# Kernel tuning notes

Hardware: AMD Instinct MI355X
Metric: run time of the kernel (lower is better)

Reference implementation:

```python
import jax, jax.numpy as jnp
import numpy as np

V, H_BASE, D, L, K = 32000, 4096, 512, 2, 4
B = 64

def setup_inputs() -> dict:
    key = jax.random.key(0)
    ks = jax.random.split(key, 12)
    s = 0.02
    return {
        "hidden_state": jax.random.normal(ks[0], (B, H_BASE), jnp.float32),
        "in_proj_w": jax.random.normal(ks[1], (D, H_BASE), jnp.float32) * s,
        "in_proj_b": jnp.zeros((D,), jnp.float32),
        "w_ih0": jax.random.normal(ks[2], (3 * D, D), jnp.float32) * s,
        "w_hh0": jax.random.normal(ks[3], (3 * D, D), jnp.float32) * s,
        "b_ih0": jax.random.normal(ks[4], (3 * D,), jnp.float32) * s,
        "b_hh0": jax.random.normal(ks[5], (3 * D,), jnp.float32) * s,
        "w_ih1": jax.random.normal(ks[6], (3 * D, D), jnp.float32) * s,
        "w_hh1": jax.random.normal(ks[7], (3 * D, D), jnp.float32) * s,
        "b_ih1": jax.random.normal(ks[8], (3 * D,), jnp.float32) * s,
        "b_hh1": jax.random.normal(ks[9], (3 * D,), jnp.float32) * s,
        "embed": jax.random.normal(ks[10], (V, D), jnp.float32) * s,
        "out_w": jax.random.normal(ks[11], (V, D), jnp.float32) * s,
    }

def _gru_cell(x, h, w_ih, w_hh, b_ih, b_hh):
    # PyTorch GRU gate order: r, z, n
    gi = x @ w_ih.T + b_ih  # [B, 3D]
    gh = h @ w_hh.T + b_hh
    ir, iz, inn = jnp.split(gi, 3, axis=-1)
    hr, hz, hn = jnp.split(gh, 3, axis=-1)
    r = jax.nn.sigmoid(ir + hr)
    z = jax.nn.sigmoid(iz + hz)
    n = jnp.tanh(inn + r * hn)
    return (1.0 - z) * n + z * h

def reference(hidden_state, in_proj_w, in_proj_b, w_ih0, w_hh0, b_ih0, b_hh0,
              w_ih1, w_hh1, b_ih1, b_hh1, embed, out_w):
    b = hidden_state.shape[0]
    h0 = hidden_state @ in_proj_w.T + in_proj_b  # [B, D]
    h_l0 = h0
    h_l1 = h0
    x = jnp.zeros((b, in_proj_w.shape[0]), hidden_state.dtype)
    all_logits = []
    for _ in range(K):
        h_l0 = _gru_cell(x, h_l0, w_ih0, w_hh0, b_ih0, b_hh0)
        h_l1 = _gru_cell(h_l0, h_l1, w_ih1, w_hh1, b_ih1, b_hh1)
        logits = h_l1 @ out_w.T  # [B, V]
        all_logits.append(logits)
        x = embed[jnp.argmax(logits, axis=-1)]  # greedy next-token embed
    return jnp.stack(all_logits, axis=1)  # [B, K, V]
```

## Files before the change

### kernel.cpp

```cpp
#include <hip/hip_runtime.h>
#include <math.h>


typedef __attribute__((ext_vector_type(8))) short short8;
typedef __attribute__((ext_vector_type(4))) float f32x4;

__device__ __forceinline__ unsigned short f2bf_rne(float x) {
    unsigned u = __float_as_uint(x);
    unsigned r = (u + 0x7fffu + ((u >> 16) & 1u)) >> 16;
    return (unsigned short)r;
}
__device__ __forceinline__ void split2(float x, unsigned short& hi, unsigned short& lo) {
    unsigned u = __float_as_uint(x);
    hi = (unsigned short)(u >> 16);
    float r = x - __uint_as_float(u & 0xffff0000u);
    lo = f2bf_rne(r);
}

__device__ __forceinline__ void store_plane(unsigned short* hiP, unsigned short* loP,
                                            int m, int d, float v) {
    int s = d >> 6, cl = (d >> 3) & 7, e = d & 7;
    int off = m * 512 + s * 64 + ((cl ^ (m & 7)) * 8) + e;
    unsigned short hi, lo; split2(v, hi, lo);
    hiP[off] = hi; loP[off] = lo;
}

__device__ __forceinline__ void gload16(const void* g, void* lds) {
    __builtin_amdgcn_global_load_lds(
        (const __attribute__((address_space(1))) unsigned int*)g,
        (__attribute__((address_space(3))) unsigned int*)lds, 16, 0, 0);
}

__device__ __forceinline__ void split_w_body(
    const float* __restrict__ W, unsigned short* __restrict__ H,
    unsigned short* __restrict__ L, size_t g, int kclog)
{
    int n  = (int)(g >> kclog);
    int c8 = (int)g & ((1 << kclog) - 1);
    const float* src = W + g * 8;
    float4 v0 = *(const float4*)src;
    float4 v1 = *(const float4*)(src + 4);
    unsigned short h[8], l[8];
    split2(v0.x,h[0],l[0]); split2(v0.y,h[1],l[1]); split2(v0.z,h[2],l[2]); split2(v0.w,h[3],l[3]);
    split2(v1.x,h[4],l[4]); split2(v1.y,h[5],l[5]); split2(v1.z,h[6],l[6]); split2(v1.w,h[7],l[7]);
    uint4 ph = make_uint4((unsigned)h[0]|((unsigned)h[1]<<16), (unsigned)h[2]|((unsigned)h[3]<<16),
                          (unsigned)h[4]|((unsigned)h[5]<<16), (unsigned)h[6]|((unsigned)h[7]<<16));
    uint4 pl = make_uint4((unsigned)l[0]|((unsigned)l[1]<<16), (unsigned)l[2]|((unsigned)l[3]<<16),
                          (unsigned)l[4]|((unsigned)l[5]<<16), (unsigned)l[6]|((unsigned)l[7]<<16));
    int nt = n >> 7, row = n & 127;
    int ksi = c8 >> 3;
    int slot = (c8 & 7) ^ (row & 7);
    int tpr = 1 << (kclog - 3);
    size_t off = ((size_t)(nt * tpr + ksi) * 128 + row) * 64 + slot * 8;
    *(uint4*)(H + off) = ph;
    *(uint4*)(L + off) = pl;
}

__global__ __launch_bounds__(256) void k_split_W(
    const float* __restrict__ W, unsigned short* __restrict__ H,
    unsigned short* __restrict__ L, int kclog)
{
    size_t g = (size_t)blockIdx.x * 256 + threadIdx.x;
    split_w_body(W, H, L, g, kclog);
}

__global__ __launch_bounds__(256) void k_split_gw(
    const float* __restrict__ w0, const float* __restrict__ w1,
    const float* __restrict__ w2, const float* __restrict__ w3,
    unsigned short* __restrict__ H, unsigned short* __restrict__ L)
{
    int mat = blockIdx.y;
    const float* W = mat == 0 ? w0 : mat == 1 ? w1 : mat == 2 ? w2 : w3;
    size_t g = (size_t)blockIdx.x * 256 + threadIdx.x;
    split_w_body(W, H + (size_t)mat * 786432, L + (size_t)mat * 786432, g, 6);
}

__global__ __launch_bounds__(256) void k_split_A(
    const float* __restrict__ hidden, char* __restrict__ hidH, char* __restrict__ hidL)
{
    int g = blockIdx.x * 256 + threadIdx.x;
    int m = g >> 9;
    int cc = g & 511;
    int s = cc >> 3, cl = cc & 7;
    const float* src = hidden + m * 4096 + cc * 8;
    float4 v0 = *(const float4*)src;
    float4 v1 = *(const float4*)(src + 4);
    unsigned short h[8], l[8];
    split2(v0.x,h[0],l[0]); split2(v0.y,h[1],l[1]); split2(v0.z,h[2],l[2]); split2(v0.w,h[3],l[3]);
    split2(v1.x,h[4],l[4]); split2(v1.y,h[5],l[5]); split2(v1.z,h[6],l[6]); split2(v1.w,h[7],l[7]);
    uint4 ph = make_uint4((unsigned)h[0]|((unsigned)h[1]<<16), (unsigned)h[2]|((unsigned)h[3]<<16),
                          (unsigned)h[4]|((unsigned)h[5]<<16), (unsigned)h[6]|((unsigned)h[7]<<16));
    uint4 pl = make_uint4((unsigned)l[0]|((unsigned)l[1]<<16), (unsigned)l[2]|((unsigned)l[3]<<16),
                          (unsigned)l[4]|((unsigned)l[5]<<16), (unsigned)l[6]|((unsigned)l[7]<<16));
    int off = m * 8192 + s * 128 + ((cl ^ (m & 7)) * 16);
    *(uint4*)(hidH + off) = ph;
    *(uint4*)(hidL + off) = pl;
}

__device__ __forceinline__ void mfma_core(
    const unsigned short* __restrict__ AsH0, const unsigned short* __restrict__ AsL0,
    const unsigned short* __restrict__ BsH0, const unsigned short* __restrict__ BsL0,
    int wv, int lr, int lh, f32x4* acc)
{
#pragma unroll
    for (int kk2 = 0; kk2 < 2; ++kk2) {
        int aoff = lr * 64 + (((kk2 * 4 + lh) ^ (lr & 7)) * 8);
        short8 ah[4], al[4];
#pragma unroll
        for (int mt = 0; mt < 4; ++mt) {
            ah[mt] = *(const short8*)(AsH0 + mt * 1024 + aoff);
            al[mt] = *(const short8*)(AsL0 + mt * 1024 + aoff);
        }
        int brow = wv * 16 + lr;
        int boff = brow * 64 + (((kk2 * 4 + lh) ^ (brow & 7)) * 8);
        short8 bh = *(const short8*)(BsH0 + boff);
        short8 bl = *(const short8*)(BsL0 + boff);
#pragma unroll
        for (int mt = 0; mt < 4; ++mt) {
            acc[mt] = __builtin_amdgcn_mfma_f32_16x16x32_bf16(ah[mt], bh, acc[mt], 0, 0, 0);
            acc[mt] = __builtin_amdgcn_mfma_f32_16x16x32_bf16(ah[mt], bl, acc[mt], 0, 0, 0);
            acc[mt] = __builtin_amdgcn_mfma_f32_16x16x32_bf16(al[mt], bh, acc[mt], 0, 0, 0);
        }
    }
}

__device__ __forceinline__ void epilogue_write(
    float* __restrict__ C, int ldc, int n0, int wv, int lr, int lh, const f32x4* acc)
{
#pragma unroll
    for (int mt = 0; mt < 4; ++mt)
#pragma unroll
        for (int i = 0; i < 4; ++i) {
            int mm = mt * 16 + lh * 4 + i;
            C[mm * ldc + n0 + wv * 16 + lr] = acc[mt][i];
        }
}

__device__ __forceinline__ void mfma_gemm(
    const char* __restrict__ AH, const char* __restrict__ AL, int AstrideB, int akk0,
    const unsigned short* __restrict__ BH, const unsigned short* __restrict__ BL,
    size_t btileU, int nk,
    float* __restrict__ C, int ldc, int n0,
    unsigned short (*AsH)[4096], unsigned short (*AsL)[4096],
    unsigned short (*BsH)[8192], unsigned short (*BsL)[8192])
{
    const int tid  = threadIdx.x;
    const int wv   = tid >> 6;
    const int lane = tid & 63;
    const int lr   = lane & 15;
    const int lh   = lane >> 4;
    const int m    = tid >> 3;
    const int cp   = tid & 7;

    f32x4 acc[4];
#pragma unroll
    for (int i = 0; i < 4; ++i) acc[i] = (f32x4){0.f, 0.f, 0.f, 0.f};

    auto stage = [&](int t, int p) {
        const int ka = (akk0 + t * 64) * 2;
        gload16(AH + m * AstrideB + ka + cp * 16, (char*)AsH[p] + wv * 1024);
        gload16(AL + m * AstrideB + ka + cp * 16, (char*)AsL[p] + wv * 1024);
        const char* bH = (const char*)BH + (btileU + (size_t)t * 8192) * 2;
        const char* bL = (const char*)BL + (btileU + (size_t)t * 8192) * 2;
        gload16(bH + wv * 2048 +        lane * 16, (char*)BsH[p] + wv * 2048);
        gload16(bH + wv * 2048 + 1024 + lane * 16, (char*)BsH[p] + wv * 2048 + 1024);
        gload16(bL + wv * 2048 +        lane * 16, (char*)BsL[p] + wv * 2048);
        gload16(bL + wv * 2048 + 1024 + lane * 16, (char*)BsL[p] + wv * 2048 + 1024);
    };

    stage(0, 0);
    __syncthreads();

    for (int t = 0; t < nk; ++t) {
        const int p = t & 1;
        if (t + 1 < nk) stage(t + 1, p ^ 1);
        mfma_core(AsH[p], AsL[p], BsH[p], BsL[p], wv, lr, lh, acc);
        __syncthreads();
    }

    epilogue_write(C, ldc, n0, wv, lr, lh, acc);
}

#define DECLARE_LDS() \
    __shared__ alignas(16) unsigned short AsH[2][4096]; \
    __shared__ alignas(16) unsigned short AsL[2][4096]; \
    __shared__ alignas(16) unsigned short BsH[2][8192]; \
    __shared__ alignas(16) unsigned short BsL[2][8192];

__global__ __launch_bounds__(512) void k_inproj(
    const char* __restrict__ hidH, const char* __restrict__ hidL,
    const unsigned short* __restrict__ WH, const unsigned short* __restrict__ WL,
    float* __restrict__ part)
{
    DECLARE_LDS();
    int nt = blockIdx.x & 3;
    int ks = blockIdx.x >> 2;
    mfma_gemm(hidH, hidL, 8192, ks * 256,
              WH, WL, (size_t)(nt * 64 + ks * 4) * 8192, 4,
              part + ks * 32768, 512, nt * 128,
              AsH, AsL, BsH, BsL);
}

__global__ __launch_bounds__(256) void k_reduce_inproj(
    const float* __restrict__ part, const float* __restrict__ bias,
    float* __restrict__ hA, float* __restrict__ hB,
    unsigned short* hAH, unsigned short* hAL,
    unsigned short* hBH, unsigned short* hBL,
    unsigned short* xH,  unsigned short* xL)
{
    int i = blockIdx.x * 256 + threadIdx.x;
    int b = i >> 9;
    int d = i & 511;
    float s = bias[d];
#pragma unroll
    for (int ks = 0; ks < 16; ++ks) s += part[ks * 32768 + i];
    hA[i] = s;
    hB[i] = s;
    store_plane(hAH, hAL, b, d, s);
    store_plane(hBH, hBL, b, d, s);
    store_plane(xH,  xL,  b, d, 0.f);
}

__global__ __launch_bounds__(512) void k_gates(
    const char* __restrict__ xH, const char* __restrict__ xL,
    const char* __restrict__ hH, const char* __restrict__ hL,
    const unsigned short* __restrict__ gwH, const unsigned short* __restrict__ gwL,
    int layer, float* __restrict__ gip, float* __restrict__ ghp)
{
    DECLARE_LDS();
    int bx  = blockIdx.x;
    int nt  = bx % 12;
    int ks  = (bx / 12) & 3;
    int mat = bx / 48;
    const char* AH = mat ? hH : xH;
    const char* AL = mat ? hL : xL;
    float* C = (mat ? ghp : gip) + ks * 98304;
    size_t btile = ((size_t)(layer * 2 + mat) * 96 + nt * 8 + ks * 2) * 8192;
    mfma_gemm(AH, AL, 1024, ks * 128,
              gwH, gwL, btile, 2,
              C, 1536, nt * 128,
              AsH, AsL, BsH, BsL);
}

__global__ __launch_bounds__(256) void k_combine(
    const float* __restrict__ gip, const float* __restrict__ ghp,
    const float* __restrict__ b_ih, const float* __restrict__ b_hh,
    float* __restrict__ h, unsigned short* hH, unsigned short* hL)
{
    int i = blockIdx.x * 256 + threadIdx.x;
    int b = i >> 9;
    int d = i & 511;
    int base = b * 1536 + d;
    float ir = b_ih[d], iz = b_ih[d + 512], inn = b_ih[d + 1024];
    float hr = b_hh[d], hz = b_hh[d + 512], hn = b_hh[d + 1024];
#pragma unroll
    for (int ks = 0; ks < 4; ++ks) {
        const float* gi = gip + ks * 98304 + base;
        const float* gh = ghp + ks * 98304 + base;
        ir  += gi[0];    iz += gi[512];  inn += gi[1024];
        hr  += gh[0];    hz += gh[512];  hn  += gh[1024];
    }
    float r = 1.f / (1.f + expf(-(ir + hr)));
    float z = 1.f / (1.f + expf(-(iz + hz)));
    float n = tanhf(inn + r * hn);
    float hv = (1.f - z) * n + z * h[i];
    h[i] = hv;
    store_plane(hH, hL, b, d, hv);
}

__global__ __launch_bounds__(256) void k_logits(
    const char* __restrict__ hBH, const char* __restrict__ hBL,
    const float* __restrict__ out_w,
    float* __restrict__ out, int step,
    float* __restrict__ pval, int* __restrict__ pidx)
{
    __shared__ alignas(16) unsigned short AsH[2][4096];
    __shared__ alignas(16) unsigned short AsL[2][4096];
    __shared__ alignas(16) unsigned short BsH[2][4096];
    __shared__ alignas(16) unsigned short BsL[2][4096];

    const int tid  = threadIdx.x;
    const int wv   = tid >> 6;
    const int lane = tid & 63;
    const int lr   = lane & 15;
    const int lh   = lane >> 4;
    const int bx   = blockIdx.x;
    const int n0   = bx * 64;

    const int ar1 = wv * 16 + (lane >> 3);
    const int acp = lane & 7;
    auto stageA = [&](int kaB, int p) {
        gload16(hBH + ar1 * 1024 + kaB + acp * 16,       (char*)AsH[p] + wv * 2048);
        gload16(hBH + (ar1 + 8) * 1024 + kaB + acp * 16, (char*)AsH[p] + wv * 2048 + 1024);
        gload16(hBL + ar1 * 1024 + kaB + acp * 16,       (char*)AsL[p] + wv * 2048);
        gload16(hBL + (ar1 + 8) * 1024 + kaB + acp * 16, (char*)AsL[p] + wv * 2048 + 1024);
    };

    const int bn = tid >> 2, bq = tid & 3;
    const float* Wb = out_w + (size_t)(n0 + bn) * 512 + bq * 16;
    const int wo0 = bn * 64 + (((2 * bq)     ^ (bn & 7)) * 8);
    const int wo1 = bn * 64 + (((2 * bq + 1) ^ (bn & 7)) * 8);

    float4 r0, r1, r2, r3;
    auto loadB = [&](int t) {
        const float* s = Wb + t * 64;
        r0 = *(const float4*)s;       r1 = *(const float4*)(s + 4);
        r2 = *(const float4*)(s + 8); r3 = *(const float4*)(s + 12);
    };
    auto writeB = [&](int p) {
        unsigned short h[16], l[16];
        split2(r0.x,h[0],l[0]);   split2(r0.y,h[1],l[1]);   split2(r0.z,h[2],l[2]);   split2(r0.w,h[3],l[3]);
        split2(r1.x,h[4],l[4]);   split2(r1.y,h[5],l[5]);   split2(r1.z,h[6],l[6]);   split2(r1.w,h[7],l[7]);
        split2(r2.x,h[8],l[8]);   split2(r2.y,h[9],l[9]);   split2(r2.z,h[10],l[10]); split2(r2.w,h[11],l[11]);
        split2(r3.x,h[12],l[12]); split2(r3.y,h[13],l[13]); split2(r3.z,h[14],l[14]); split2(r3.w,h[15],l[15]);
        *(uint4*)(BsH[p] + wo0) = make_uint4(
            (unsigned)h[0]|((unsigned)h[1]<<16),  (unsigned)h[2]|((unsigned)h[3]<<16),
            (unsigned)h[4]|((unsigned)h[5]<<16),  (unsigned)h[6]|((unsigned)h[7]<<16));
        *(uint4*)(BsH[p] + wo1) = make_uint4(
            (unsigned)h[8]|((unsigned)h[9]<<16),  (unsigned)h[10]|((unsigned)h[11]<<16),
            (unsigned)h[12]|((unsigned)h[13]<<16),(unsigned)h[14]|((unsigned)h[15]<<16));
        *(uint4*)(BsL[p] + wo0) = make_uint4(
            (unsigned)l[0]|((unsigned)l[1]<<16),  (unsigned)l[2]|((unsigned)l[3]<<16),
            (unsigned)l[4]|((unsigned)l[5]<<16),  (unsigned)l[6]|((unsigned)l[7]<<16));
        *(uint4*)(BsL[p] + wo1) = make_uint4(
            (unsigned)l[8]|((unsigned)l[9]<<16),  (unsigned)l[10]|((unsigned)l[11]<<16),
            (unsigned)l[12]|((unsigned)l[13]<<16),(unsigned)l[14]|((unsigned)l[15]<<16));
    };

    f32x4 acc[4];
#pragma unroll
    for (int i = 0; i < 4; ++i) acc[i] = (f32x4){0.f, 0.f, 0.f, 0.f};

    loadB(0);
    stageA(0, 0);
    writeB(0);
    __syncthreads();
#pragma unroll
    for (int t = 0; t < 8; ++t) {
        const int p = t & 1;
        if (t < 7) { loadB(t + 1); stageA((t + 1) * 128, p ^ 1); }
        mfma_core(AsH[p], AsL[p], BsH[p], BsL[p], wv, lr, lh, acc);
        if (t < 7) writeB(p ^ 1);
        __syncthreads();
    }

    epilogue_write(out + step * 32000, 128000, n0, wv, lr, lh, acc);

    float* sv = (float*)&AsH[0][0];
    int*   sc = (int*)&AsL[0][0];
#pragma unroll
    for (int mt = 0; mt < 4; ++mt)
#pragma unroll
        for (int i = 0; i < 4; ++i) {
            float v = acc[mt][i];
            int   c = n0 + wv * 16 + lr;
#pragma unroll
            for (int msk = 1; msk < 16; msk <<= 1) {
                float ov = __shfl_xor(v, msk, 64);
                int   oc = __shfl_xor(c, msk, 64);
                if (ov > v || (ov == v && oc < c)) { v = ov; c = oc; }
            }
            if (lr == 0) {
                int row = mt * 16 + lh * 4 + i;
                sv[wv * 64 + row] = v;
                sc[wv * 64 + row] = c;
            }
        }
    __syncthreads();
    if (tid < 64) {
        float v = sv[tid]; int c = sc[tid];
#pragma unroll
        for (int w = 1; w < 4; ++w) {
            float ov = sv[w * 64 + tid]; int oc = sc[w * 64 + tid];
            if (ov > v || (ov == v && oc < c)) { v = ov; c = oc; }
        }
        pval[bx * 64 + tid] = v;
        pidx[bx * 64 + tid] = c;
    }
}

__global__ __launch_bounds__(256) void k_reduce_embed(
    const float* __restrict__ pval, const int* __restrict__ pidx,
    const float* __restrict__ embed, unsigned short* xH, unsigned short* xL)
{
    __shared__ float sv[256];
    __shared__ int   sc[256];
    const int b = blockIdx.x;
    const int tid = threadIdx.x;
    float v = pval[tid * 64 + b];
    int   c = pidx[tid * 64 + b];
    if (tid + 256 < 500) {
        float ov = pval[(tid + 256) * 64 + b];
        int   oc = pidx[(tid + 256) * 64 + b];
        if (ov > v || (ov == v && oc < c)) { v = ov; c = oc; }
    }
    sv[tid] = v; sc[tid] = c;
    __syncthreads();
    for (int s = 128; s > 0; s >>= 1) {
        if (tid < s) {
            float ov = sv[tid + s]; int oc = sc[tid + s];
            if (ov > sv[tid] || (ov == sv[tid] && oc < sc[tid])) { sv[tid] = ov; sc[tid] = oc; }
        }
        __syncthreads();
    }
    int tok = sc[0];
    for (int j = tid; j < 512; j += 256)
        store_plane(xH, xL, b, j, embed[(size_t)tok * 512 + j]);
}

extern "C" void kernel_launch(void* const* d_in, const int* in_sizes, int n_in,
                              void* d_out, int out_size, void* d_ws, size_t ws_size,
                              hipStream_t stream)
{
    const float* hidden = (const float*)d_in[0];
    const float* in_w   = (const float*)d_in[1];
    const float* in_b   = (const float*)d_in[2];
    const float* w_ih0  = (const float*)d_in[3];
    const float* w_hh0  = (const float*)d_in[4];
    const float* b_ih0  = (const float*)d_in[5];
    const float* b_hh0  = (const float*)d_in[6];
    const float* w_ih1  = (const float*)d_in[7];
    const float* w_hh1  = (const float*)d_in[8];
    const float* b_ih1  = (const float*)d_in[9];
    const float* b_hh1  = (const float*)d_in[10];
    const float* embed  = (const float*)d_in[11];
    const float* out_w  = (const float*)d_in[12];
    float* out = (float*)d_out;
    char*  ws  = (char*)d_ws;

    float* hA  = (float*)(ws + 0);
    float* hB  = (float*)(ws + 131072);
    unsigned short* xH  = (unsigned short*)(ws + 262144);
    unsigned short* xL  = (unsigned short*)(ws + 327680);
    unsigned short* hAH = (unsigned short*)(ws + 393216);
    unsigned short* hAL = (unsigned short*)(ws + 458752);
    unsigned short* hBH = (unsigned short*)(ws + 524288);
    unsigned short* hBL = (unsigned short*)(ws + 589824);
    char* hidH = ws + 655360;
    char* hidL = ws + 1179648;
    float* gip = (float*)(ws + 1703936);
    float* ghp = (float*)(ws + 3276800);
    float* pval = (float*)(ws + 4849664);
    int*   pidx = (int*)  (ws + 4980736);
    float* ipart = (float*)(ws + 5111808);
    unsigned short* gwH = (unsigned short*)(ws + 7208960);
    unsigned short* gwL = (unsigned short*)(ws + 13500416);
    unsigned short* inH = (unsigned short*)(ws + 19791872);
    unsigned short* inL = (unsigned short*)(ws + 23986176);

    k_split_A<<<128, 256, 0, stream>>>(hidden, hidH, hidL);
    k_split_gw<<<dim3(384, 4), 256, 0, stream>>>(w_ih0, w_hh0, w_ih1, w_hh1, gwH, gwL);
    k_split_W<<<1024, 256, 0, stream>>>(in_w, inH, inL, 9);
    k_inproj<<<64, 512, 0, stream>>>(hidH, hidL, inH, inL, ipart);
    k_reduce_inproj<<<128, 256, 0, stream>>>(ipart, in_b, hA, hB,
                                             hAH, hAL, hBH, hBL, xH, xL);

    for (int step = 0; step < 4; ++step) {
        k_gates<<<96, 512, 0, stream>>>((char*)xH, (char*)xL, (char*)hAH, (char*)hAL,
                                        gwH, gwL, 0, gip, ghp);
        k_combine<<<128, 256, 0, stream>>>(gip, ghp, b_ih0, b_hh0, hA, hAH, hAL);
        k_gates<<<96, 512, 0, stream>>>((char*)hAH, (char*)hAL, (char*)hBH, (char*)hBL,
                                        gwH, gwL, 1, gip, ghp);
        k_combine<<<128, 256, 0, stream>>>(gip, ghp, b_ih1, b_hh1, hB, hBH, hBL);
        k_logits<<<500, 256, 0, stream>>>((char*)hBH, (char*)hBL, out_w,
                                          out, step, pval, pidx);
        k_reduce_embed<<<64, 256, 0, stream>>>(pval, pidx, embed, xH, xL);
    }
}
```

Baseline: 357.8 us.

## Fuse argmax reduction and embedding gather into layer-0 gate GEMM, merge split kernels

The three weight/activation split kernels become one launch. The separate argmax-reduce plus embed kernel is removed: each layer-0 input-gate block now reduces the per-block argmax partials itself, gathers the embedding rows, splits them to bf16 hi/lo and writes them straight into LDS. At step 0 the x@W_ih product is skipped and zeros are written instead. This cuts several launches per step and the x plane round trip through global memory, at the cost of every gate block redundantly redoing the 500-way argmax reduction.

```diff
diff --git a/kernel.cpp b/kernel.cpp
--- a/kernel.cpp
+++ b/kernel.cpp
@@ -56,29 +56,10 @@
     *(uint4*)(L + off) = pl;
 }
 
-__global__ __launch_bounds__(256) void k_split_W(
-    const float* __restrict__ W, unsigned short* __restrict__ H,
-    unsigned short* __restrict__ L, int kclog)
-{
-    size_t g = (size_t)blockIdx.x * 256 + threadIdx.x;
-    split_w_body(W, H, L, g, kclog);
-}
-
-__global__ __launch_bounds__(256) void k_split_gw(
-    const float* __restrict__ w0, const float* __restrict__ w1,
-    const float* __restrict__ w2, const float* __restrict__ w3,
-    unsigned short* __restrict__ H, unsigned short* __restrict__ L)
-{
-    int mat = blockIdx.y;
-    const float* W = mat == 0 ? w0 : mat == 1 ? w1 : mat == 2 ? w2 : w3;
-    size_t g = (size_t)blockIdx.x * 256 + threadIdx.x;
-    split_w_body(W, H + (size_t)mat * 786432, L + (size_t)mat * 786432, g, 6);
-}
-
-__global__ __launch_bounds__(256) void k_split_A(
-    const float* __restrict__ hidden, char* __restrict__ hidH, char* __restrict__ hidL)
-{
-    int g = blockIdx.x * 256 + threadIdx.x;
+__device__ __forceinline__ void split_a_body(
+    const float* __restrict__ hidden, char* __restrict__ hidH,
+    char* __restrict__ hidL, int g)
+{
     int m = g >> 9;
     int cc = g & 511;
     int s = cc >> 3, cl = cc & 7;
@@ -97,6 +78,28 @@
     *(uint4*)(hidL + off) = pl;
 }
 
+__global__ __launch_bounds__(256) void k_split_all(
+    const float* __restrict__ w_ih0, const float* __restrict__ w_hh0,
+    const float* __restrict__ w_ih1, const float* __restrict__ w_hh1,
+    const float* __restrict__ in_w, const float* __restrict__ hidden,
+    unsigned short* __restrict__ gwH, unsigned short* __restrict__ gwL,
+    unsigned short* __restrict__ inH, unsigned short* __restrict__ inL,
+    char* __restrict__ hidH, char* __restrict__ hidL)
+{
+    size_t u = (size_t)blockIdx.x * 256 + threadIdx.x;
+    if (u < 393216) {
+        int mat = (int)(u / 98304);
+        const float* W = mat == 0 ? w_ih0 : mat == 1 ? w_hh0
+                       : mat == 2 ? w_ih1 : w_hh1;
+        split_w_body(W, gwH + (size_t)mat * 786432, gwL + (size_t)mat * 786432,
+                     u % 98304, 6);
+    } else if (u < 655360) {
+        split_w_body(in_w, inH, inL, u - 393216, 9);
+    } else {
+        split_a_body(hidden, hidH, hidL, (int)(u - 655360));
+    }
+}
+
 __device__ __forceinline__ void mfma_core(
     const unsigned short* __restrict__ AsH0, const unsigned short* __restrict__ AsL0,
     const unsigned short* __restrict__ BsH0, const unsigned short* __restrict__ BsL0,
@@ -205,8 +208,7 @@
     const float* __restrict__ part, const float* __restrict__ bias,
     float* __restrict__ hA, float* __restrict__ hB,
     unsigned short* hAH, unsigned short* hAL,
-    unsigned short* hBH, unsigned short* hBL,
-    unsigned short* xH,  unsigned short* xL)
+    unsigned short* hBH, unsigned short* hBL)
 {
     int i = blockIdx.x * 256 + threadIdx.x;
     int b = i >> 9;
@@ -218,24 +220,114 @@
     hB[i] = s;
     store_plane(hAH, hAL, b, d, s);
     store_plane(hBH, hBL, b, d, s);
-    store_plane(xH,  xL,  b, d, 0.f);
-}
-
-__global__ __launch_bounds__(512) void k_gates(
-    const char* __restrict__ xH, const char* __restrict__ xL,
-    const char* __restrict__ hH, const char* __restrict__ hL,
+}
+
+__global__ __launch_bounds__(512) void k_gates_l0(
+    int step,
+    const float* __restrict__ pval, const int* __restrict__ pidx,
+    const float* __restrict__ embed,
+    const char* __restrict__ hAH, const char* __restrict__ hAL,
     const unsigned short* __restrict__ gwH, const unsigned short* __restrict__ gwL,
-    int layer, float* __restrict__ gip, float* __restrict__ ghp)
+    float* __restrict__ gip, float* __restrict__ ghp)
+{
+    DECLARE_LDS();
+    __shared__ int stok[64];
+    const int bx = blockIdx.x, tid = threadIdx.x;
+    const int nt = bx % 12, ks = (bx / 12) & 3, mat = bx / 48;
+
+    if (mat) {
+        size_t btile = ((size_t)96 + nt * 8 + ks * 2) * 8192;
+        mfma_gemm(hAH, hAL, 1024, ks * 128, gwH, gwL, btile, 2,
+                  ghp + ks * 98304, 1536, nt * 128, AsH, AsL, BsH, BsL);
+        return;
+    }
+
+    float* C = gip + ks * 98304;
+    if (step == 0) {
+        float4 z = make_float4(0.f, 0.f, 0.f, 0.f);
+        for (int q = tid; q < 2048; q += 512) {
+            int r2 = q >> 5, cq = q & 31;
+            *(float4*)(C + r2 * 1536 + nt * 128 + cq * 4) = z;
+        }
+        return;
+    }
+
+    const int wv = tid >> 6, lane = tid & 63, lr = lane & 15, lh = lane >> 4;
+    const size_t btileU = ((size_t)(nt * 8 + ks * 2)) * 8192;
+    auto stageB = [&](int t, int p) {
+        const char* bH = (const char*)gwH + (btileU + (size_t)t * 8192) * 2;
+        const char* bL = (const char*)gwL + (btileU + (size_t)t * 8192) * 2;
+        gload16(bH + wv * 2048 +        lane * 16, (char*)BsH[p] + wv * 2048);
+        gload16(bH + wv * 2048 + 1024 + lane * 16, (char*)BsH[p] + wv * 2048 + 1024);
+        gload16(bL + wv * 2048 +        lane * 16, (char*)BsL[p] + wv * 2048);
+        gload16(bL + wv * 2048 + 1024 + lane * 16, (char*)BsL[p] + wv * 2048 + 1024);
+    };
+
+    stageB(0, 0);
+
+    {
+        int r = tid >> 3, j0 = tid & 7;
+        float v = -3.4e38f; int c = 0x7fffffff;
+        for (int j = j0; j < 500; j += 8) {
+            float ov = pval[j * 64 + r]; int oc = pidx[j * 64 + r];
+            if (ov > v || (ov == v && oc < c)) { v = ov; c = oc; }
+        }
+#pragma unroll
+        for (int msk = 1; msk < 8; msk <<= 1) {
+            float ov = __shfl_xor(v, msk, 64);
+            int   oc = __shfl_xor(c, msk, 64);
+            if (ov > v || (ov == v && oc < c)) { v = ov; c = oc; }
+        }
+        if (j0 == 0) stok[r] = c;
+    }
+    __syncthreads();
+
+    {
+        int mm = tid >> 3, cp = tid & 7;
+        int tok = stok[mm];
+        int off = mm * 64 + ((cp ^ (mm & 7)) * 8);
+#pragma unroll
+        for (int t2 = 0; t2 < 2; ++t2) {
+            const float* src = embed + (size_t)tok * 512 + ks * 128 + t2 * 64 + cp * 8;
+            float4 v0 = *(const float4*)src;
+            float4 v1 = *(const float4*)(src + 4);
+            unsigned short h[8], l[8];
+            split2(v0.x,h[0],l[0]); split2(v0.y,h[1],l[1]); split2(v0.z,h[2],l[2]); split2(v0.w,h[3],l[3]);
+            split2(v1.x,h[4],l[4]); split2(v1.y,h[5],l[5]); split2(v1.z,h[6],l[6]); split2(v1.w,h[7],l[7]);
+            uint4 ph = make_uint4((unsigned)h[0]|((unsigned)h[1]<<16), (unsigned)h[2]|((unsigned)h[3]<<16),
+                                  (unsigned)h[4]|((unsigned)h[5]<<16), (unsigned)h[6]|((unsigned)h[7]<<16));
+            uint4 pl = make_uint4((unsigned)l[0]|((unsigned)l[1]<<16), (unsigned)l[2]|((unsigned)l[3]<<16),
+                                  (unsigned)l[4]|((unsigned)l[5]<<16), (unsigned)l[6]|((unsigned)l[7]<<16));
+            *(uint4*)(AsH[t2] + off) = ph;
+            *(uint4*)(AsL[t2] + off) = pl;
+        }
+    }
+    stageB(1, 1);
+    __syncthreads();
+
+    f32x4 acc[4];
+#pragma unroll
+    for (int i = 0; i < 4; ++i) acc[i] = (f32x4){0.f, 0.f, 0.f, 0.f};
+    mfma_core(AsH[0], AsL[0], BsH[0], BsL[0], wv, lr, lh, acc);
+    mfma_core(AsH[1], AsL[1], BsH[1], BsL[1], wv, lr, lh, acc);
+    epilogue_write(C, 1536, nt * 128, wv, lr, lh, acc);
+}
+
+__global__ __launch_bounds__(512) void k_gates_l1(
+    const char* __restrict__ hAH, const char* __restrict__ hAL,
+    const char* __restrict__ hBH, const char* __restrict__ hBL,
+    const unsigned short* __restrict__ gwH, const unsigned short* __restrict__ gwL,
+    float* __restrict__ gip, float* __restrict__ ghp)
 {
     DECLARE_LDS();
     int bx  = blockIdx.x;
     int nt  = bx % 12;
     int ks  = (bx / 12) & 3;
     int mat = bx / 48;
-    const char* AH = mat ? hH : xH;
-    const char* AL = mat ? hL : xL;
+    const char* AH = mat ? hBH : hAH;
+    const char* AL = mat ? hBL : hAL;
     float* C = (mat ? ghp : gip) + ks * 98304;
-    size_t btile = ((size_t)(layer * 2 + mat) * 96 + nt * 8 + ks * 2) * 8192;
+    size_t btile = ((size_t)(2 + mat) * 96 + nt * 8 + ks * 2) * 8192;
     mfma_gemm(AH, AL, 1024, ks * 128,
               gwH, gwL, btile, 2,
               C, 1536, nt * 128,
@@ -379,35 +471,6 @@
     }
 }
 
-__global__ __launch_bounds__(256) void k_reduce_embed(
-    const float* __restrict__ pval, const int* __restrict__ pidx,
-    const float* __restrict__ embed, unsigned short* xH, unsigned short* xL)
-{
-    __shared__ float sv[256];
-    __shared__ int   sc[256];
-    const int b = blockIdx.x;
-    const int tid = threadIdx.x;
-    float v = pval[tid * 64 + b];
-    int   c = pidx[tid * 64 + b];
-    if (tid + 256 < 500) {
-        float ov = pval[(tid + 256) * 64 + b];
-        int   oc = pidx[(tid + 256) * 64 + b];
-        if (ov > v || (ov == v && oc < c)) { v = ov; c = oc; }
-    }
-    sv[tid] = v; sc[tid] = c;
-    __syncthreads();
-    for (int s = 128; s > 0; s >>= 1) {
-        if (tid < s) {
-            float ov = sv[tid + s]; int oc = sc[tid + s];
-            if (ov > sv[tid] || (ov == sv[tid] && oc < sc[tid])) { sv[tid] = ov; sc[tid] = oc; }
-        }
-        __syncthreads();
-    }
-    int tok = sc[0];
-    for (int j = tid; j < 512; j += 256)
-        store_plane(xH, xL, b, j, embed[(size_t)tok * 512 + j]);
-}
-
 extern "C" void kernel_launch(void* const* d_in, const int* in_sizes, int n_in,
                               void* d_out, int out_size, void* d_ws, size_t ws_size,
                               hipStream_t stream)
@@ -430,8 +493,6 @@
 
     float* hA  = (float*)(ws + 0);
     float* hB  = (float*)(ws + 131072);
-    unsigned short* xH  = (unsigned short*)(ws + 262144);
-    unsigned short* xL  = (unsigned short*)(ws + 327680);
     unsigned short* hAH = (unsigned short*)(ws + 393216);
     unsigned short* hAL = (unsigned short*)(ws + 458752);
     unsigned short* hBH = (unsigned short*)(ws + 524288);
@@ -448,22 +509,23 @@
     unsigned short* inH = (unsigned short*)(ws + 19791872);
     unsigned short* inL = (unsigned short*)(ws + 23986176);
 
-    k_split_A<<<128, 256, 0, stream>>>(hidden, hidH, hidL);
-    k_split_gw<<<dim3(384, 4), 256, 0, stream>>>(w_ih0, w_hh0, w_ih1, w_hh1, gwH, gwL);
-    k_split_W<<<1024, 256, 0, stream>>>(in_w, inH, inL, 9);
+    k_split_all<<<2688, 256, 0, stream>>>(w_ih0, w_hh0, w_ih1, w_hh1,
+                                          in_w, hidden,
+                                          gwH, gwL, inH, inL, hidH, hidL);
     k_inproj<<<64, 512, 0, stream>>>(hidH, hidL, inH, inL, ipart);
     k_reduce_inproj<<<128, 256, 0, stream>>>(ipart, in_b, hA, hB,
-                                             hAH, hAL, hBH, hBL, xH, xL);
+                                             hAH, hAL, hBH, hBL);
 
     for (int step = 0; step < 4; ++step) {
-        k_gates<<<96, 512, 0, stream>>>((char*)xH, (char*)xL, (char*)hAH, (char*)hAL,
-                                        gwH, gwL, 0, gip, ghp);
+        k_gates_l0<<<96, 512, 0, stream>>>(step, pval, pidx, embed,
+                                           (char*)hAH, (char*)hAL,
+                                           gwH, gwL, gip, ghp);
         k_combine<<<128, 256, 0, stream>>>(gip, ghp, b_ih0, b_hh0, hA, hAH, hAL);
-        k_gates<<<96, 512, 0, stream>>>((char*)hAH, (char*)hAL, (char*)hBH, (char*)hBL,
-                                        gwH, gwL, 1, gip, ghp);
+        k_gates_l1<<<96, 512, 0, stream>>>((char*)hAH, (char*)hAL,
+                                           (char*)hBH, (char*)hBL,
+                                           gwH, gwL, gip, ghp);
         k_combine<<<128, 256, 0, stream>>>(gip, ghp, b_ih1, b_hh1, hB, hBH, hBL);
         k_logits<<<500, 256, 0, stream>>>((char*)hBH, (char*)hBL, out_w,
                                           out, step, pval, pidx);
-        k_reduce_embed<<<64, 256, 0, stream>>>(pval, pidx, embed, xH, xL);
-    }
-}
+    }
+}
```

Result: slower. 393.2 us (+9.9%).
